# Performance work log

Measured on AMD Instinct MI355X. Metric: run time of the kernel, lower is better.

The kernel has to match this reference:

```python
import jax, jax.numpy as jnp
import numpy as np


def _hamming(n):
    # torch.hamming_window(n, periodic=False): 0.54 - 0.46*cos(2*pi*i/(n-1))
    if n == 1:
        return jnp.ones((1,), jnp.float32)
    i = jnp.arange(n, dtype=jnp.float32)
    return 0.54 - 0.46 * jnp.cos(2.0 * jnp.pi * i / (n - 1))


def setup_inputs() -> dict:
    key = jax.random.key(0)
    k1, k2, k3 = jax.random.split(key, 3)
    N, CIN, COUT, K = 4, 16, 32, 3
    D, H, W = 16, 64, 64
    x = jax.random.normal(k1, (N, CIN, D, H, W), dtype=jnp.float32)
    # Conv3d default init: U(-1/sqrt(fan_in), 1/sqrt(fan_in)), fan_in = cin*k^3
    bound = 1.0 / np.sqrt(CIN * K * K * K)
    weight = jax.random.uniform(k2, (COUT, CIN, K, K, K), jnp.float32, -bound, bound)
    bias = jax.random.uniform(k3, (COUT,), jnp.float32, -bound, bound)
    gamma = jnp.ones((COUT,), jnp.float32)   # BatchNorm3d weight
    beta = jnp.zeros((COUT,), jnp.float32)   # BatchNorm3d bias
    return {"x": x, "weight": weight, "bias": bias, "gamma": gamma, "beta": beta}


def reference(x, weight, bias, gamma, beta):
    # --- shrink_conv_weights: per-(cout,cin) soft-threshold, fully vectorized ---
    cutoff = weight.max(axis=(2, 3, 4), keepdims=True) * 0.5          # [cout,cin,1,1,1]
    shrunk = jnp.sign(weight) * jax.nn.relu(jnp.abs(weight) - cutoff / 100.0)
    w = jnp.where(weight < cutoff, shrunk, weight)
    # --- hamming window over the 3 kernel dims ---
    kd, kh, kw = w.shape[2], w.shape[3], w.shape[4]
    win = _hamming(kd)[:, None, None] * _hamming(kh)[None, :, None] * _hamming(kw)[None, None, :]
    w = w * win[None, None]                                           # [cout,cin,kd,kh,kw]
    # --- conv3d, padding='same' ---
    y = jax.lax.conv_general_dilated(
        x, w, window_strides=(1, 1, 1), padding="SAME",
        dimension_numbers=("NCDHW", "OIDHW", "NCDHW"))
    y = y + bias[None, :, None, None, None]
    # --- BatchNorm3d (training mode: batch stats, biased variance, eps=1e-5) ---
    mean = y.mean(axis=(0, 2, 3, 4), keepdims=True)
    var = y.var(axis=(0, 2, 3, 4), keepdims=True)
    y = (y - mean) * jax.lax.rsqrt(var + 1e-5)
    y = y * gamma[None, :, None, None, None] + beta[None, :, None, None, None]
    # --- softplus nonlinearity ---
    return jax.nn.softplus(y)
```

## Files before the change

### kernel.cpp

```cpp
#include <hip/hip_runtime.h>
#include <math.h>

#define N_    4
#define CIN   16
#define COUT  32
#define DD    16
#define HH_   64
#define WW_   64
#define MCNT  262144.0f

typedef __attribute__((ext_vector_type(8))) short short8;
typedef __attribute__((ext_vector_type(4))) float floatx4;

__device__ __forceinline__ ushort f2bf(float f) {
    uint u = __float_as_uint(f);
    uint r = (u + 0x7fffu + ((u >> 16) & 1u)) >> 16;
    return (ushort)r;
}
__device__ __forceinline__ float bf2f(ushort v) {
    return __uint_as_float(((uint)v) << 16);
}
__device__ __forceinline__ float softplus_f(float z) {
    return fmaxf(z, 0.0f) + log1pf(expf(-fabsf(z)));
}

#define FAST_XT_F    0
#define FAST_WB_F    2162688
#define FAST_SC_F    2169856
#define FAST_PART_F  2169920
#define FAST_YB_F    2235456
#define FAST_BYTES_FP32Y  ((size_t)FAST_YB_F * 4)
#define FAST_BYTES_BF16Y  ((size_t)(FAST_YB_F + 4194304) * 4)
#define XROW_U16     1056
#define XROW_CHUNKS  132
#define WROW_U16     40

__global__ __launch_bounds__(512, 4)
void conv_direct(const float* __restrict__ x, const float* __restrict__ weight,
                 const float* __restrict__ bias, ushort* __restrict__ yb,
                 float* __restrict__ part) {
    __shared__ ushort xs[18 * XROW_U16];
    __shared__ ushort wlds[14 * COUT * WROW_U16];
    __shared__ float sred[8][64];

    int b = blockIdx.x;
    int n = b >> 8, d = (b >> 4) & 15, h0 = (b & 15) * 4;
    int t = threadIdx.x;
    int l = t & 63;
    int wv_ = t >> 6;
    int hq = wv_ >> 1, cf = wv_ & 1;
    int h = h0 + hq;
    int s = l & 15, g = l >> 4;
    int ghi = g >> 1;

    ((float*)sred)[t] = 0.0f;

    {
        int cout = t >> 4, cin = t & 15;
        const float* wp = weight + (cout * CIN + cin) * 27;
        float wv[27];
        float mx = -INFINITY;
        #pragma unroll
        for (int k = 0; k < 27; ++k) { wv[k] = wp[k]; mx = fmaxf(mx, wv[k]); }
        float cutoff = mx * 0.5f;
        const float win[3] = {0.08f, 1.0f, 0.08f};
        #pragma unroll
        for (int k = 0; k < 27; ++k) {
            float w = wv[k];
            float sg = (w > 0.0f) ? 1.0f : ((w < 0.0f) ? -1.0f : 0.0f);
            float shr = sg * fmaxf(fabsf(w) - cutoff * 0.01f, 0.0f);
            float o = (w < cutoff) ? shr : w;
            int kd = k / 9, kr = k % 9, kh = kr / 3, kw = kr % 3;
            o *= win[kd] * win[kh] * win[kw];
            int q = (kd * 3 + kh) * 3 + kw;
            int grp = q >> 1, half = q & 1;
            wlds[(grp * COUT + cout) * WROW_U16 + half * 16 + cin] = f2bf(o);
        }
        wlds[(13 * COUT + cout) * WROW_U16 + 16 + cin] = 0;
    }

    for (int i = t; i < 18 * 2; i += 512) {
        int row = i >> 1, cq = i & 1;
        uint4 z = {0u, 0u, 0u, 0u};
        *(uint4*)&xs[row * XROW_U16 + 0 * 16 + cq * 8]  = z;
        *(uint4*)&xs[row * XROW_U16 + 65 * 16 + cq * 8] = z;
    }
    const int CSTRIDE = DD * HH_ * WW_;
    for (int i = t; i < 2304; i += 512) {
        int row = i >> 7;
        int rem = i & 127;
        int cq = rem >> 6;
        int w  = rem & 63;
        int zdi = row / 6, rh = row - zdi * 6;
        int zd = d - 1 + zdi, zh = h0 - 1 + rh;
        uint4 pk = {0u, 0u, 0u, 0u};
        if ((unsigned)zd < DD && (unsigned)zh < HH_) {
            const float* p0 = x + (((size_t)(n * CIN + cq * 8) * DD + zd) * HH_ + zh) * WW_ + w;
            float v0 = p0[0 * CSTRIDE], v1 = p0[1 * CSTRIDE];
            float v2 = p0[2 * CSTRIDE], v3 = p0[3 * CSTRIDE];
            float v4 = p0[4 * CSTRIDE], v5 = p0[5 * CSTRIDE];
            float v6 = p0[6 * CSTRIDE], v7 = p0[7 * CSTRIDE];
            pk.x = (uint)f2bf(v0) | ((uint)f2bf(v1) << 16);
            pk.y = (uint)f2bf(v2) | ((uint)f2bf(v3) << 16);
            pk.z = (uint)f2bf(v4) | ((uint)f2bf(v5) << 16);
            pk.w = (uint)f2bf(v6) | ((uint)f2bf(v7) << 16);
        }
        *(uint4*)&xs[row * XROW_U16 + (w + 1) * 16 + cq * 8] = pk;
    }
    __syncthreads();

    short8 A[14];
    #pragma unroll
    for (int grp = 0; grp < 14; ++grp)
        A[grp] = *(const short8*)&wlds[(grp * COUT + cf * 16 + s) * WROW_U16 + g * 8];

    floatx4 acc[4];
    #pragma unroll
    for (int wf = 0; wf < 4; ++wf) acc[wf] = (floatx4){0.f, 0.f, 0.f, 0.f};

    int hbase = hq * XROW_U16 + s * 16 + (g & 1) * 8;

    #pragma unroll
    for (int grp = 0; grp < 14; ++grp) {
        const int qa = 2 * grp;
        const int qb = (grp == 13) ? 26 : 2 * grp + 1;
        const int t9a = qa / 3, t9b = qb / 3;
        const int ca = ((t9a / 3) * 6 + (t9a % 3)) * XROW_U16 + (qa % 3) * 16;
        const int cb = ((t9b / 3) * 6 + (t9b % 3)) * XROW_U16 + (qb % 3) * 16;
        int baddr = hbase + (ghi ? cb : ca);
        #pragma unroll
        for (int wf = 0; wf < 4; ++wf) {
            short8 B = *(const short8*)&xs[baddr + wf * 256];
            acc[wf] = __builtin_amdgcn_mfma_f32_16x16x32_bf16(A[grp], B, acc[wf], 0, 0, 0);
        }
    }

    float s1[4], s2[4];
    #pragma unroll
    for (int j = 0; j < 4; ++j) { s1[j] = 0.f; s2[j] = 0.f; }
    #pragma unroll
    for (int j = 0; j < 4; ++j) {
        int co = cf * 16 + g * 4 + j;
        float bval = bias[co];
        size_t obase = ((size_t)(n * COUT + co) * DD + d) * (HH_ * WW_) + h * WW_ + s;
        #pragma unroll
        for (int wf = 0; wf < 4; ++wf) {
            float val = acc[wf][j] + bval;
            yb[obase + wf * 16] = f2bf(val);
            s1[j] += val;
            s2[j] += val * val;
        }
    }
    #pragma unroll
    for (int m = 1; m < 16; m <<= 1) {
        #pragma unroll
        for (int j = 0; j < 4; ++j) {
            s1[j] += __shfl_xor(s1[j], m);
            s2[j] += __shfl_xor(s2[j], m);
        }
    }
    if (s == 0) {
        #pragma unroll
        for (int j = 0; j < 4; ++j) {
            int co = cf * 16 + g * 4 + j;
            sred[wv_][co]      = s1[j];
            sred[wv_][32 + co] = s2[j];
        }
    }
    __syncthreads();
    if (t < 64) {
        int cfh = (t >> 4) & 1;
        float v = sred[cfh][t] + sred[2 + cfh][t] + sred[4 + cfh][t] + sred[6 + cfh][t];
        part[(size_t)b * 64 + t] = v;
    }
}

__global__ __launch_bounds__(1024)
void stats_fast(const float* __restrict__ part, const float* __restrict__ gamma,
                const float* __restrict__ beta, float* __restrict__ scale,
                float* __restrict__ shift) {
    __shared__ float red[16][64];
    __shared__ float tot[64];
    int t = threadIdx.x;
    int c = t & 63, rg = t >> 6;
    const float* p = part + (size_t)rg * 64 * 64 + c;
    float s = 0.f;
    #pragma unroll 8
    for (int b = 0; b < 64; ++b) s += p[b * 64];
    red[rg][c] = s;
    __syncthreads();
    if (t < 64) {
        float v = 0.f;
        #pragma unroll
        for (int r = 0; r < 16; ++r) v += red[r][t];
        tot[t] = v;
    }
    __syncthreads();
    if (t < 32) {
        float mean = tot[t] / MCNT;
        float var  = tot[32 + t] / MCNT - mean * mean;
        float rstd = rsqrtf(var + 1e-5f);
        float sc = gamma[t] * rstd;
        scale[t] = sc;
        shift[t] = beta[t] - mean * sc;
    }
}

__global__ __launch_bounds__(256)
void bn_act_bf16(const ushort* __restrict__ yb, float* __restrict__ out,
                 const float* __restrict__ scale, const float* __restrict__ shift) {
    const int NV8 = (N_ * COUT * DD * HH_ * WW_) / 8;
    int stride = gridDim.x * blockDim.x;
    const short8* y8 = (const short8*)yb;
    for (int i = blockIdx.x * blockDim.x + threadIdx.x; i < NV8; i += stride) {
        int ch = (i >> 13) & 31;
        float sc = scale[ch];
        float sh = shift[ch];
        short8 yv = y8[i];
        float4 o0, o1;
        float* op0 = (float*)&o0;
        float* op1 = (float*)&o1;
        #pragma unroll
        for (int j = 0; j < 4; ++j) {
            float z = bf2f((ushort)yv[j]) * sc + sh;
            op0[j] = softplus_f(z);
        }
        #pragma unroll
        for (int j = 0; j < 4; ++j) {
            float z = bf2f((ushort)yv[4 + j]) * sc + sh;
            op1[j] = softplus_f(z);
        }
        *(float4*)&out[(size_t)i * 8]     = o0;
        *(float4*)&out[(size_t)i * 8 + 4] = o1;
    }
}

__global__ __launch_bounds__(256, 4)
void transpose_prep(const float* __restrict__ x, const float* __restrict__ weight,
                    ushort* __restrict__ xt, ushort* __restrict__ wb) {
    __shared__ ushort lds[4 * 64 * 16];
    int b = blockIdx.x;
    int n = b >> 8, d = (b >> 4) & 15, h0 = (b & 15) * 4;
    int t = threadIdx.x;

    if (b == 0) {
        #pragma unroll
        for (int rep = 0; rep < 2; ++rep) {
            int p = t + rep * 256;
            int cout = p >> 4, cin = p & 15;
            const float* wp = weight + (cout * CIN + cin) * 27;
            float wv[27];
            float mx = -INFINITY;
            #pragma unroll
            for (int k = 0; k < 27; ++k) { wv[k] = wp[k]; mx = fmaxf(mx, wv[k]); }
            float cutoff = mx * 0.5f;
            const float win[3] = {0.08f, 1.0f, 0.08f};
            #pragma unroll
            for (int k = 0; k < 27; ++k) {
                float w = wv[k];
                float sg = (w > 0.0f) ? 1.0f : ((w < 0.0f) ? -1.0f : 0.0f);
                float shr = sg * fmaxf(fabsf(w) - cutoff * 0.01f, 0.0f);
                float o = (w < cutoff) ? shr : w;
                int kd = k / 9, kr = k % 9, kh = kr / 3, kw = kr % 3;
                o *= win[kd] * win[kh] * win[kw];
                int q = (kd * 3 + kh) * 3 + kw;
                int grp = q >> 1, half = q & 1;
                wb[(grp * COUT + cout) * 32 + half * 16 + cin] = f2bf(o);
            }
            wb[(13 * COUT + cout) * 32 + 16 + cin] = 0;
        }
    }

    int hh = t >> 6, w = t & 63;
    const float* xp = x + ((size_t)(n * CIN * DD + d) * HH_ + (h0 + hh)) * WW_ + w;
    const int CSTRIDE = DD * HH_ * WW_;
    uint rowv[8];
    #pragma unroll
    for (int cp = 0; cp < 8; ++cp) {
        float a  = xp[(2 * cp)     * CSTRIDE];
        float b2 = xp[(2 * cp + 1) * CSTRIDE];
        rowv[cp] = (uint)f2bf(a) | ((uint)f2bf(b2) << 16);
    }
    #pragma unroll
    for (int cp = 0; cp < 8; ++cp)
        *(uint*)&lds[(hh * 64 + w) * 16 + 2 * cp] = rowv[cp];
    __syncthreads();
    uint* xtg = (uint*)xt;
    for (int i = t; i < 4 * 528; i += 256) {
        int hh2 = i / 528, u = i - hh2 * 528;
        int slot = u >> 3, cp = u & 7;
        uint val = 0;
        if (slot >= 1 && slot <= 64)
            val = *(uint*)&lds[(hh2 * 64 + (slot - 1)) * 16 + 2 * cp];
        xtg[(size_t)((n * DD + d) * HH_ + (h0 + hh2)) * 528 + u] = val;
    }
}

__global__ __launch_bounds__(512, 4)
void conv_mfma_f32y(const ushort* __restrict__ xt, const ushort* __restrict__ wb,
                    const float* __restrict__ bias, float* __restrict__ outf,
                    float* __restrict__ part) {
    __shared__ ushort xs[18 * XROW_U16];
    __shared__ float sred[8][64];

    int b = blockIdx.x;
    int n = b >> 8, d = (b >> 4) & 15, h0 = (b & 15) * 4;
    int t = threadIdx.x;
    int l = t & 63;
    int wv_ = t >> 6;
    int hq = wv_ >> 1, cf = wv_ & 1;
    int h = h0 + hq;
    int s = l & 15, g = l >> 4;
    int ghi = g >> 1;

    ((float*)sred)[t] = 0.0f;

    short8 A[14];
    #pragma unroll
    for (int grp = 0; grp < 14; ++grp)
        A[grp] = *(const short8*)&wb[(grp * COUT + cf * 16 + s) * 32 + g * 8];

    const uint4* xt4 = (const uint4*)xt;
    uint4* xs4 = (uint4*)xs;
    for (int i = t; i < 18 * XROW_CHUNKS; i += 512) {
        int row = i / XROW_CHUNKS, c = i - row * XROW_CHUNKS;
        int zdi = row / 6, rh = row - zdi * 6;
        int zd = d - 1 + zdi, zh = h0 - 1 + rh;
        uint4 v = {0u, 0u, 0u, 0u};
        if ((unsigned)zd < DD && (unsigned)zh < HH_)
            v = xt4[(size_t)((n * DD + zd) * HH_ + zh) * XROW_CHUNKS + c];
        xs4[i] = v;
    }
    __syncthreads();

    floatx4 acc[4];
    #pragma unroll
    for (int wf = 0; wf < 4; ++wf) acc[wf] = (floatx4){0.f, 0.f, 0.f, 0.f};

    int hbase = hq * XROW_U16 + s * 16 + (g & 1) * 8;

    #pragma unroll
    for (int grp = 0; grp < 14; ++grp) {
        const int qa = 2 * grp;
        const int qb = (grp == 13) ? 26 : 2 * grp + 1;
        const int t9a = qa / 3, t9b = qb / 3;
        const int ca = ((t9a / 3) * 6 + (t9a % 3)) * XROW_U16 + (qa % 3) * 16;
        const int cb = ((t9b / 3) * 6 + (t9b % 3)) * XROW_U16 + (qb % 3) * 16;
        int baddr = hbase + (ghi ? cb : ca);
        #pragma unroll
        for (int wf = 0; wf < 4; ++wf) {
            short8 B = *(const short8*)&xs[baddr + wf * 256];
            acc[wf] = __builtin_amdgcn_mfma_f32_16x16x32_bf16(A[grp], B, acc[wf], 0, 0, 0);
        }
    }

    float s1[4], s2[4];
    #pragma unroll
    for (int j = 0; j < 4; ++j) { s1[j] = 0.f; s2[j] = 0.f; }
    #pragma unroll
    for (int j = 0; j < 4; ++j) {
        int co = cf * 16 + g * 4 + j;
        float bval = bias[co];
        size_t obase = ((size_t)(n * COUT + co) * DD + d) * (HH_ * WW_) + h * WW_ + s;
        #pragma unroll
        for (int wf = 0; wf < 4; ++wf) {
            float val = acc[wf][j] + bval;
            outf[obase + wf * 16] = val;
            s1[j] += val;
            s2[j] += val * val;
        }
    }
    #pragma unroll
    for (int m = 1; m < 16; m <<= 1) {
        #pragma unroll
        for (int j = 0; j < 4; ++j) {
            s1[j] += __shfl_xor(s1[j], m);
            s2[j] += __shfl_xor(s2[j], m);
        }
    }
    if (s == 0) {
        #pragma unroll
        for (int j = 0; j < 4; ++j) {
            int co = cf * 16 + g * 4 + j;
            sred[wv_][co]      = s1[j];
            sred[wv_][32 + co] = s2[j];
        }
    }
    __syncthreads();
    if (t < 64) {
        int cfh = (t >> 4) & 1;
        float v = sred[cfh][t] + sred[2 + cfh][t] + sred[4 + cfh][t] + sred[6 + cfh][t];
        part[(size_t)b * 64 + t] = v;
    }
}

__global__ void bn_act_kernel(float* __restrict__ out, const float* __restrict__ scale,
                              const float* __restrict__ shift) {
    const int NV4 = (N_ * COUT * DD * HH_ * WW_) / 4;
    int stride = gridDim.x * blockDim.x;
    float4* o4 = (float4*)out;
    for (int i = blockIdx.x * blockDim.x + threadIdx.x; i < NV4; i += stride) {
        int ch = (i >> 14) & 31;
        float sc = scale[ch];
        float sh = shift[ch];
        float4 val = o4[i];
        float* vp = (float*)&val;
        #pragma unroll
        for (int j = 0; j < 4; ++j) {
            float z = vp[j] * sc + sh;
            vp[j] = softplus_f(z);
        }
        o4[i] = val;
    }
}

#define WS_W      0
#define WS_SUM    13824
#define WS_SUMSQ  13856
#define WS_SCALE  13888
#define WS_SHIFT  13920

__global__ void prep_weights(const float* __restrict__ weight, float* __restrict__ ws) {
    int t = threadIdx.x;
    if (t < 64) ws[WS_SUM + t] = 0.0f;
    int cout = t >> 4, cin = t & 15;
    const float* wp = weight + (cout * CIN + cin) * 27;
    float wv[27];
    float mx = -INFINITY;
    #pragma unroll
    for (int k = 0; k < 27; ++k) { wv[k] = wp[k]; mx = fmaxf(mx, wv[k]); }
    float cutoff = mx * 0.5f;
    const float win[3] = {0.08f, 1.0f, 0.08f};
    #pragma unroll
    for (int k = 0; k < 27; ++k) {
        float w = wv[k];
        float s = (w > 0.0f) ? 1.0f : ((w < 0.0f) ? -1.0f : 0.0f);
        float shr = s * fmaxf(fabsf(w) - cutoff * 0.01f, 0.0f);
        float o = (w < cutoff) ? shr : w;
        int kd = k / 9, kr = k % 9, kh = kr / 3, kw = kr % 3;
        o *= win[kd] * win[kh] * win[kw];
        ws[WS_W + (cin * 27 + k) * COUT + cout] = o;
    }
}

#define RS 68
__global__ __launch_bounds__(256, 4)
void conv_kernel(const float* __restrict__ x, const float* __restrict__ bias,
                 const float* __restrict__ wsw, float* __restrict__ out,
                 float* __restrict__ sums, float* __restrict__ sumsqs) {
    __shared__ float xsf[3 * 6 * RS];
    __shared__ float sredf[16][8];
    int b = blockIdx.x;
    int n  = b >> 8;
    int d  = (b >> 4) & 15;
    int h0 = (b & 15) << 2;
    int tid = threadIdx.x;
    int wg = tid & 15;
    int cg2 = (tid >> 4) & 3;
    int v  = tid >> 6;
    int cohalf = v & 1;
    int hhalf  = v >> 1;
    int w0 = wg * 4;
    int co0 = cohalf * 16 + cg2 * 4;
    float acc[4][2][4];
    #pragma unroll
    for (int c = 0; c < 4; ++c)
        #pragma unroll
        for (int i = 0; i < 2; ++i)
            #pragma unroll
            for (int j = 0; j < 4; ++j) acc[c][i][j] = 0.0f;
    const float* xn = x + (size_t)n * CIN * DD * HH_ * WW_;
    for (int cin = 0; cin < CIN; ++cin) {
        __syncthreads();
        const float* xc = xn + cin * DD * HH_ * WW_;
        for (int idx = tid; idx < 3 * 6 * RS; idx += 256) {
            int row = idx / RS;
            int c   = idx - row * RS;
            int dd  = row / 6;
            int r   = row - dd * 6;
            int zd = d - 1 + dd;
            int zh = h0 - 1 + r;
            int w  = c - 1;
            float val = 0.0f;
            if ((unsigned)zd < DD && (unsigned)zh < HH_ && (unsigned)w < WW_)
                val = xc[(zd * HH_ + zh) * WW_ + w];
            xsf[idx] = val;
        }
        __syncthreads();
        const float* wc = wsw + cin * 27 * COUT + co0;
        #pragma unroll 1
        for (int kd = 0; kd < 3; ++kd) {
            float4 wvv[9];
            #pragma unroll
            for (int j = 0; j < 9; ++j)
                wvv[j] = *(const float4*)&wc[(kd * 9 + j) * COUT];
            const float* xp = &xsf[(kd * 6 + hhalf * 2) * RS];
            #pragma unroll
            for (int rr = 0; rr < 4; ++rr) {
                const float* xr_ = &xp[rr * RS + w0];
                float4 xm = *(const float4*)xr_;
                float x4 = xr_[4];
                float x5 = xr_[5];
                float xv[6] = {xm.x, xm.y, xm.z, xm.w, x4, x5};
                #pragma unroll
                for (int kh = 0; kh < 3; ++kh) {
                    int i = rr - kh;
                    if (i < 0 || i > 1) continue;
                    #pragma unroll
                    for (int kw = 0; kw < 3; ++kw) {
                        float4 w4 = wvv[kh * 3 + kw];
                        #pragma unroll
                        for (int j = 0; j < 4; ++j) {
                            float xx = xv[j + kw];
                            acc[0][i][j] = fmaf(w4.x, xx, acc[0][i][j]);
                            acc[1][i][j] = fmaf(w4.y, xx, acc[1][i][j]);
                            acc[2][i][j] = fmaf(w4.z, xx, acc[2][i][j]);
                            acc[3][i][j] = fmaf(w4.w, xx, acc[3][i][j]);
                        }
                    }
                }
            }
        }
    }
    float s1[4], s2[4];
    #pragma unroll
    for (int c = 0; c < 4; ++c) {
        float bval = bias[co0 + c];
        s1[c] = 0.0f; s2[c] = 0.0f;
        #pragma unroll
        for (int i = 0; i < 2; ++i) {
            float4 o;
            float* op = (float*)&o;
            #pragma unroll
            for (int j = 0; j < 4; ++j) {
                float val = acc[c][i][j] + bval;
                op[j] = val;
                s1[c] += val;
                s2[c] += val * val;
            }
            int hh = h0 + hhalf * 2 + i;
            *(float4*)&out[((((size_t)n * COUT + co0 + c) * DD + d) * HH_ + hh) * WW_ + w0] = o;
        }
    }
    #pragma unroll
    for (int m = 1; m < 16; m <<= 1) {
        #pragma unroll
        for (int c = 0; c < 4; ++c) {
            s1[c] += __shfl_xor(s1[c], m);
            s2[c] += __shfl_xor(s2[c], m);
        }
    }
    if ((tid & 15) == 0) {
        int gg = tid >> 4;
        #pragma unroll
        for (int c = 0; c < 4; ++c) { sredf[gg][c] = s1[c]; sredf[gg][4 + c] = s2[c]; }
    }
    __syncthreads();
    if (tid < 64) {
        int co   = tid & 31;
        int kind = tid >> 5;
        int ch   = (co >> 4) & 1;
        int cgg  = (co >> 2) & 3;
        int c    = co & 3;
        float val = sredf[ch * 4 + cgg][kind * 4 + c] + sredf[(ch + 2) * 4 + cgg][kind * 4 + c];
        atomicAdd(kind ? &sumsqs[co] : &sums[co], val);
    }
}

__global__ void stats_kernel(const float* __restrict__ gamma, const float* __restrict__ beta,
                             const float* __restrict__ sums, const float* __restrict__ sumsqs,
                             float* __restrict__ scale, float* __restrict__ shift) {
    int c = threadIdx.x;
    if (c >= 32) return;
    float mean = sums[c] / MCNT;
    float var  = sumsqs[c] / MCNT - mean * mean;
    float rstd = rsqrtf(var + 1e-5f);
    float sc = gamma[c] * rstd;
    scale[c] = sc;
    shift[c] = beta[c] - mean * sc;
}

extern "C" void kernel_launch(void* const* d_in, const int* in_sizes, int n_in,
                              void* d_out, int out_size, void* d_ws, size_t ws_size,
                              hipStream_t stream) {
    const float* x      = (const float*)d_in[0];
    const float* weight = (const float*)d_in[1];
    const float* bias   = (const float*)d_in[2];
    const float* gamma  = (const float*)d_in[3];
    const float* beta   = (const float*)d_in[4];
    float* out = (float*)d_out;
    float* wsf = (float*)d_ws;

    float* scale = wsf + FAST_SC_F;
    float* shift = wsf + FAST_SC_F + 32;
    float* part  = wsf + FAST_PART_F;

    if (ws_size >= FAST_BYTES_BF16Y) {
        ushort* yb = (ushort*)(wsf + FAST_YB_F);
        hipLaunchKernelGGL(conv_direct, dim3(1024), dim3(512), 0, stream,
                           x, weight, bias, yb, part);
        hipLaunchKernelGGL(stats_fast, dim3(1), dim3(1024), 0, stream,
                           part, gamma, beta, scale, shift);
        hipLaunchKernelGGL(bn_act_bf16, dim3(2048), dim3(256), 0, stream,
                           yb, out, scale, shift);
    } else if (ws_size >= FAST_BYTES_FP32Y) {
        ushort* xt = (ushort*)(wsf + FAST_XT_F);
        ushort* wb = (ushort*)(wsf + FAST_WB_F);
        hipLaunchKernelGGL(transpose_prep, dim3(1024), dim3(256), 0, stream,
                           x, weight, xt, wb);
        hipLaunchKernelGGL(conv_mfma_f32y, dim3(1024), dim3(512), 0, stream,
                           xt, wb, bias, out, part);
        hipLaunchKernelGGL(stats_fast, dim3(1), dim3(1024), 0, stream,
                           part, gamma, beta, scale, shift);
        hipLaunchKernelGGL(bn_act_kernel, dim3(2048), dim3(256), 0, stream,
                           out, scale, shift);
    } else {
        hipLaunchKernelGGL(prep_weights, dim3(1), dim3(512), 0, stream, weight, wsf);
        hipLaunchKernelGGL(conv_kernel, dim3(1024), dim3(256), 0, stream,
                           x, bias, wsf + WS_W, out, wsf + WS_SUM, wsf + WS_SUMSQ);
        hipLaunchKernelGGL(stats_kernel, dim3(1), dim3(64), 0, stream,
                           gamma, beta, wsf + WS_SUM, wsf + WS_SUMSQ, wsf + WS_SCALE, wsf + WS_SHIFT);
        hipLaunchKernelGGL(bn_act_kernel, dim3(2048), dim3(256), 0, stream,
                           out, wsf + WS_SCALE, wsf + WS_SHIFT);
    }
}
```

Measured before the change: 54.35 us.

## Precompute bf16 weights once and halve conv block tile to two rows

Weight shrinking, windowing and bf16 packing move into a separate single-block prep kernel that writes to workspace. Each conv block no longer redoes this per block and loads its MFMA A operands straight from global memory. The conv tile drops from 4 to 2 output rows with 256 threads, giving 2048 blocks and a smaller LDS footprint, and the stats kernel is templated on the partial-sum count. The cost is one extra launch and more halo re-reads of x, since each block now loads 4 input rows to produce 2 output rows instead of 6 for 4.

```diff
diff --git a/kernel.cpp b/kernel.cpp
--- a/kernel.cpp
+++ b/kernel.cpp
@@ -28,23 +28,46 @@
 #define FAST_WB_F    2162688
 #define FAST_SC_F    2169856
 #define FAST_PART_F  2169920
-#define FAST_YB_F    2235456
+#define FAST_YB_F    2301056
 #define FAST_BYTES_FP32Y  ((size_t)FAST_YB_F * 4)
 #define FAST_BYTES_BF16Y  ((size_t)(FAST_YB_F + 4194304) * 4)
 #define XROW_U16     1056
 #define XROW_CHUNKS  132
-#define WROW_U16     40
-
-__global__ __launch_bounds__(512, 4)
-void conv_direct(const float* __restrict__ x, const float* __restrict__ weight,
-                 const float* __restrict__ bias, ushort* __restrict__ yb,
-                 float* __restrict__ part) {
-    __shared__ ushort xs[18 * XROW_U16];
-    __shared__ ushort wlds[14 * COUT * WROW_U16];
-    __shared__ float sred[8][64];
+
+__global__ void prep_w(const float* __restrict__ weight, ushort* __restrict__ wb) {
+    int t = threadIdx.x;
+    int cout = t >> 4, cin = t & 15;
+    const float* wp = weight + (cout * CIN + cin) * 27;
+    float wv[27];
+    float mx = -INFINITY;
+    #pragma unroll
+    for (int k = 0; k < 27; ++k) { wv[k] = wp[k]; mx = fmaxf(mx, wv[k]); }
+    float cutoff = mx * 0.5f;
+    const float win[3] = {0.08f, 1.0f, 0.08f};
+    #pragma unroll
+    for (int k = 0; k < 27; ++k) {
+        float w = wv[k];
+        float sg = (w > 0.0f) ? 1.0f : ((w < 0.0f) ? -1.0f : 0.0f);
+        float shr = sg * fmaxf(fabsf(w) - cutoff * 0.01f, 0.0f);
+        float o = (w < cutoff) ? shr : w;
+        int kd = k / 9, kr = k % 9, kh = kr / 3, kw = kr % 3;
+        o *= win[kd] * win[kh] * win[kw];
+        int q = (kd * 3 + kh) * 3 + kw;
+        int grp = q >> 1, half = q & 1;
+        wb[(grp * COUT + cout) * 32 + half * 16 + cin] = f2bf(o);
+    }
+    wb[(13 * COUT + cout) * 32 + 16 + cin] = 0;
+}
+
+__global__ __launch_bounds__(256, 4)
+void conv256(const float* __restrict__ x, const ushort* __restrict__ wb,
+             const float* __restrict__ bias, ushort* __restrict__ yb,
+             float* __restrict__ part) {
+    __shared__ ushort xs[12 * XROW_U16];
+    __shared__ float sred[4][64];
 
     int b = blockIdx.x;
-    int n = b >> 8, d = (b >> 4) & 15, h0 = (b & 15) * 4;
+    int n = b >> 9, d = (b >> 5) & 15, h0 = (b & 31) * 2;
     int t = threadIdx.x;
     int l = t & 63;
     int wv_ = t >> 6;
@@ -55,43 +78,24 @@
 
     ((float*)sred)[t] = 0.0f;
 
-    {
-        int cout = t >> 4, cin = t & 15;
-        const float* wp = weight + (cout * CIN + cin) * 27;
-        float wv[27];
-        float mx = -INFINITY;
-        #pragma unroll
-        for (int k = 0; k < 27; ++k) { wv[k] = wp[k]; mx = fmaxf(mx, wv[k]); }
-        float cutoff = mx * 0.5f;
-        const float win[3] = {0.08f, 1.0f, 0.08f};
-        #pragma unroll
-        for (int k = 0; k < 27; ++k) {
-            float w = wv[k];
-            float sg = (w > 0.0f) ? 1.0f : ((w < 0.0f) ? -1.0f : 0.0f);
-            float shr = sg * fmaxf(fabsf(w) - cutoff * 0.01f, 0.0f);
-            float o = (w < cutoff) ? shr : w;
-            int kd = k / 9, kr = k % 9, kh = kr / 3, kw = kr % 3;
-            o *= win[kd] * win[kh] * win[kw];
-            int q = (kd * 3 + kh) * 3 + kw;
-            int grp = q >> 1, half = q & 1;
-            wlds[(grp * COUT + cout) * WROW_U16 + half * 16 + cin] = f2bf(o);
-        }
-        wlds[(13 * COUT + cout) * WROW_U16 + 16 + cin] = 0;
-    }
-
-    for (int i = t; i < 18 * 2; i += 512) {
-        int row = i >> 1, cq = i & 1;
+    short8 A[14];
+    #pragma unroll
+    for (int grp = 0; grp < 14; ++grp)
+        A[grp] = *(const short8*)&wb[(grp * COUT + cf * 16 + s) * 32 + g * 8];
+
+    if (t < 24) {
+        int row = t >> 1, cq = t & 1;
         uint4 z = {0u, 0u, 0u, 0u};
         *(uint4*)&xs[row * XROW_U16 + 0 * 16 + cq * 8]  = z;
         *(uint4*)&xs[row * XROW_U16 + 65 * 16 + cq * 8] = z;
     }
     const int CSTRIDE = DD * HH_ * WW_;
-    for (int i = t; i < 2304; i += 512) {
+    for (int i = t; i < 1536; i += 256) {
         int row = i >> 7;
         int rem = i & 127;
         int cq = rem >> 6;
         int w  = rem & 63;
-        int zdi = row / 6, rh = row - zdi * 6;
+        int zdi = row >> 2, rh = row & 3;
         int zd = d - 1 + zdi, zh = h0 - 1 + rh;
         uint4 pk = {0u, 0u, 0u, 0u};
         if ((unsigned)zd < DD && (unsigned)zh < HH_) {
@@ -109,11 +113,6 @@
     }
     __syncthreads();
 
-    short8 A[14];
-    #pragma unroll
-    for (int grp = 0; grp < 14; ++grp)
-        A[grp] = *(const short8*)&wlds[(grp * COUT + cf * 16 + s) * WROW_U16 + g * 8];
-
     floatx4 acc[4];
     #pragma unroll
     for (int wf = 0; wf < 4; ++wf) acc[wf] = (floatx4){0.f, 0.f, 0.f, 0.f};
@@ -125,8 +124,8 @@
         const int qa = 2 * grp;
         const int qb = (grp == 13) ? 26 : 2 * grp + 1;
         const int t9a = qa / 3, t9b = qb / 3;
-        const int ca = ((t9a / 3) * 6 + (t9a % 3)) * XROW_U16 + (qa % 3) * 16;
-        const int cb = ((t9b / 3) * 6 + (t9b % 3)) * XROW_U16 + (qb % 3) * 16;
+        const int ca = ((t9a / 3) * 4 + (t9a % 3)) * XROW_U16 + (qa % 3) * 16;
+        const int cb = ((t9b / 3) * 4 + (t9b % 3)) * XROW_U16 + (qb % 3) * 16;
         int baddr = hbase + (ghi ? cb : ca);
         #pragma unroll
         for (int wf = 0; wf < 4; ++wf) {
@@ -170,23 +169,25 @@
     __syncthreads();
     if (t < 64) {
         int cfh = (t >> 4) & 1;
-        float v = sred[cfh][t] + sred[2 + cfh][t] + sred[4 + cfh][t] + sred[6 + cfh][t];
+        float v = sred[cfh][t] + sred[2 + cfh][t];
         part[(size_t)b * 64 + t] = v;
     }
 }
 
+template <int NBLK>
 __global__ __launch_bounds__(1024)
-void stats_fast(const float* __restrict__ part, const float* __restrict__ gamma,
-                const float* __restrict__ beta, float* __restrict__ scale,
-                float* __restrict__ shift) {
+void stats_fast_t(const float* __restrict__ part, const float* __restrict__ gamma,
+                  const float* __restrict__ beta, float* __restrict__ scale,
+                  float* __restrict__ shift) {
     __shared__ float red[16][64];
     __shared__ float tot[64];
+    const int RPG = NBLK / 16;
     int t = threadIdx.x;
     int c = t & 63, rg = t >> 6;
-    const float* p = part + (size_t)rg * 64 * 64 + c;
+    const float* p = part + (size_t)rg * RPG * 64 + c;
     float s = 0.f;
     #pragma unroll 8
-    for (int b = 0; b < 64; ++b) s += p[b * 64];
+    for (int r = 0; r < RPG; ++r) s += p[r * 64];
     red[rg][c] = s;
     __syncthreads();
     if (t < 64) {
@@ -594,23 +595,24 @@
     float* scale = wsf + FAST_SC_F;
     float* shift = wsf + FAST_SC_F + 32;
     float* part  = wsf + FAST_PART_F;
+    ushort* wb   = (ushort*)(wsf + FAST_WB_F);
 
     if (ws_size >= FAST_BYTES_BF16Y) {
         ushort* yb = (ushort*)(wsf + FAST_YB_F);
-        hipLaunchKernelGGL(conv_direct, dim3(1024), dim3(512), 0, stream,
-                           x, weight, bias, yb, part);
-        hipLaunchKernelGGL(stats_fast, dim3(1), dim3(1024), 0, stream,
+        hipLaunchKernelGGL(prep_w, dim3(1), dim3(512), 0, stream, weight, wb);
+        hipLaunchKernelGGL(conv256, dim3(2048), dim3(256), 0, stream,
+                           x, wb, bias, yb, part);
+        hipLaunchKernelGGL((stats_fast_t<2048>), dim3(1), dim3(1024), 0, stream,
                            part, gamma, beta, scale, shift);
         hipLaunchKernelGGL(bn_act_bf16, dim3(2048), dim3(256), 0, stream,
                            yb, out, scale, shift);
     } else if (ws_size >= FAST_BYTES_FP32Y) {
         ushort* xt = (ushort*)(wsf + FAST_XT_F);
-        ushort* wb = (ushort*)(wsf + FAST_WB_F);
         hipLaunchKernelGGL(transpose_prep, dim3(1024), dim3(256), 0, stream,
                            x, weight, xt, wb);
         hipLaunchKernelGGL(conv_mfma_f32y, dim3(1024), dim3(512), 0, stream,
                            xt, wb, bias, out, part);
-        hipLaunchKernelGGL(stats_fast, dim3(1), dim3(1024), 0, stream,
+        hipLaunchKernelGGL((stats_fast_t<1024>), dim3(1), dim3(1024), 0, stream,
                            part, gamma, beta, scale, shift);
         hipLaunchKernelGGL(bn_act_kernel, dim3(2048), dim3(256), 0, stream,
                            out, scale, shift);
```

After: 62.18 us. 14.4% more time.
